# Kernel optimization log

Hardware: AMD Instinct MI355X
Metric: run time of the kernel (lower is better)

Reference implementation:

```python
import jax, jax.numpy as jnp
import numpy as np

B = 65536
QUERY_DIM = 1024
CROSS_DIM = 1024
HEADS = 16
DIM_HEAD = 64
INNER = HEADS * DIM_HEAD  # 1024
SCALE = DIM_HEAD ** -0.5


def setup_inputs() -> dict:
    key = jax.random.key(0)
    ks = jax.random.split(key, 7)
    s_in = 1.0 / np.sqrt(QUERY_DIM)
    s_c = 1.0 / np.sqrt(CROSS_DIM)
    s_o = 1.0 / np.sqrt(INNER)
    return {
        "latent": jax.random.normal(ks[0], (B, QUERY_DIM), jnp.float32),
        "cond_latent": jax.random.normal(ks[1], (B, CROSS_DIM), jnp.float32),
        "Wq": jax.random.normal(ks[2], (INNER, QUERY_DIM), jnp.float32) * s_in,
        "Wk": jax.random.normal(ks[3], (INNER, CROSS_DIM), jnp.float32) * s_c,
        "Wv": jax.random.normal(ks[4], (INNER, CROSS_DIM), jnp.float32) * s_c,
        "Wout": jax.random.normal(ks[5], (QUERY_DIM, INNER), jnp.float32) * s_o,
        "bout": jax.random.normal(ks[6], (QUERY_DIM,), jnp.float32) * s_o,
    }


def reference(latent, cond_latent, Wq, Wk, Wv, Wout, bout):
    # projections: [B, inner] -> [B, heads, dim_head]
    Q = (latent @ Wq.T).reshape(B, HEADS, DIM_HEAD)
    K = (cond_latent @ Wk.T).reshape(B, HEADS, DIM_HEAD)
    V = (cond_latent @ Wv.T).reshape(B, HEADS, DIM_HEAD)
    # attention across the heads axis: scores [B, heads, heads]
    scores = jnp.einsum("bhd,bgd->bhg", Q, K) * SCALE
    probs = jax.nn.softmax(scores, axis=-1)
    feats = jnp.einsum("bhg,bgd->bhd", probs, V).reshape(B, INNER)
    return feats @ Wout.T + bout
```

## Files before the change

### kernel.cpp

```cpp
#include <hip/hip_runtime.h>
#include <hip/hip_bf16.h>

#define NB    65536
#define KDIM  1024
#define NDIM  1024

#define BM 256
#define BN 256
#define BK 64
#define NT (KDIM / BK)

typedef float f32x4 __attribute__((ext_vector_type(4)));
typedef short short8 __attribute__((ext_vector_type(8)));
typedef unsigned short ushort8v __attribute__((ext_vector_type(8)));

static __device__ __forceinline__ unsigned short f2bf(float f) {
    union { float f; unsigned u; } v; v.f = f;
    unsigned r = v.u + 0x7FFFu + ((v.u >> 16) & 1u);
    return (unsigned short)(r >> 16);
}
static __device__ __forceinline__ float bf2f(unsigned short h) {
    union { unsigned u; float f; } v; v.u = ((unsigned)h) << 16;
    return v.f;
}

static __device__ __forceinline__ void gload16(const unsigned short* g, unsigned short* l) {
    __builtin_amdgcn_global_load_lds(
        (const __attribute__((address_space(1))) unsigned int*)g,
        (__attribute__((address_space(3))) unsigned int*)l, 16, 0, 0);
}

__global__ __launch_bounds__(256) void f32_to_bf16_k(
    const float* __restrict__ s, unsigned short* __restrict__ d, int n4)
{
    const int stride = gridDim.x * 256;
    for (int i = blockIdx.x * 256 + threadIdx.x; i < n4; i += stride) {
        float4 v = reinterpret_cast<const float4*>(s)[i];
        ushort4 o;
        o.x = f2bf(v.x); o.y = f2bf(v.y); o.z = f2bf(v.z); o.w = f2bf(v.w);
        reinterpret_cast<ushort4*>(d)[i] = o;
    }
}

template<int OUT_F32>
__global__ __launch_bounds__(512, 2) void gemm256(
    const unsigned short* __restrict__ Ap, const unsigned short* __restrict__ Wp,
    const float* __restrict__ bias, void* __restrict__ Cptr)
{
    constexpr int N = NDIM;
    constexpr int GN = NDIM / BN;
    __shared__ alignas(16) unsigned short lds[2][2][32][512];

    const int t    = threadIdx.x;
    const int lane = t & 63;
    const int wid  = t >> 6;
    const int wm   = wid >> 2;
    const int wn   = wid & 3;

    const int nwg  = gridDim.x;
    const int cpx  = nwg >> 3;
    const int orig = blockIdx.x;
    const int wgid = (orig & 7) * cpx + (orig >> 3);
    const int bn0  = (wgid & (GN - 1)) * BN;
    const int bm0  = (wgid / GN) * BM;

    const size_t aoff = (size_t)(lane & 15) * KDIM + (lane >> 4) * 8;

#define FENCE_ asm volatile("" ::: "memory")
#define BAR_   do { FENCE_; __builtin_amdgcn_s_barrier(); FENCE_; } while (0)
#define VMBAR_ do { asm volatile("s_waitcnt vmcnt(8)" ::: "memory");            \
                    __builtin_amdgcn_s_barrier(); FENCE_; } while (0)

#define LDA_(BUF, MI, KS) \
    (*reinterpret_cast<const short8*>(&lds[BUF][0][(wm * 8 + (MI)) * 2 + (KS)][lane * 8]))
#define LDB_(BUF, NI, KS) \
    (*reinterpret_cast<const short8*>(&lds[BUF][1][(wn * 4 + (NI)) * 2 + (KS)][lane * 8]))

#define STAGE_(TAU, SLOT, AB, KS) do {                                          \
        int _tc = (TAU) < NT ? (TAU) : NT - 1;    \
        const unsigned short* _b = (AB) ? Wp : Ap;                              \
        int _r0 = (AB) ? bn0 : bm0;                                             \
        _Pragma("unroll")                                                       \
        for (int _j = 0; _j < 2; ++_j) {                                        \
            int _f = wid * 2 + _j;                                              \
            gload16(_b + (size_t)(_r0 + _f * 16) * KDIM + _tc * BK + (KS) * 32 + aoff, \
                    &lds[SLOT][AB][_f * 2 + (KS)][0]);                          \
        }                                                                       \
    } while (0)

#define MFMA_(ACCB, AF) do { _Pragma("unroll")                                  \
    for (int mi = 0; mi < 4; ++mi) {                                            \
        acc[(ACCB) + mi][0] = __builtin_amdgcn_mfma_f32_16x16x32_bf16(AF[mi], bq0, acc[(ACCB) + mi][0], 0, 0, 0); \
        acc[(ACCB) + mi][1] = __builtin_amdgcn_mfma_f32_16x16x32_bf16(AF[mi], bq1, acc[(ACCB) + mi][1], 0, 0, 0); \
        acc[(ACCB) + mi][2] = __builtin_amdgcn_mfma_f32_16x16x32_bf16(AF[mi], bq2, acc[(ACCB) + mi][2], 0, 0, 0); \
        acc[(ACCB) + mi][3] = __builtin_amdgcn_mfma_f32_16x16x32_bf16(AF[mi], bq3, acc[(ACCB) + mi][3], 0, 0, 0); \
    } } while (0)

#define GROUP_(BUF, OBUF, TT) do {                                              \
                                                   \
        _Pragma("unroll")                                                       \
        for (int mi = 0; mi < 4; ++mi) afA[mi] = LDA_(BUF, mi, 0);              \
        bq0 = LDB_(BUF, 0, 0); bq1 = LDB_(BUF, 1, 0);                           \
        bq2 = LDB_(BUF, 2, 0); bq3 = LDB_(BUF, 3, 0);                           \
        STAGE_((TT) + 1, OBUF, 0, 1);                                           \
        BAR_;                                                                   \
        __builtin_amdgcn_s_setprio(1); MFMA_(0, afA); __builtin_amdgcn_s_setprio(0); \
        BAR_;                                                                   \
                                                   \
        _Pragma("unroll")                                                       \
        for (int mi = 0; mi < 4; ++mi) afB[mi] = LDA_(BUF, 4 + mi, 0);          \
        STAGE_((TT) + 1, OBUF, 1, 1);                                           \
        VMBAR_;                                                                 \
        __builtin_amdgcn_s_setprio(1); MFMA_(4, afB); __builtin_amdgcn_s_setprio(0); \
        BAR_;                                                                   \
                                                   \
        _Pragma("unroll")                                                       \
        for (int mi = 0; mi < 4; ++mi) afA[mi] = LDA_(BUF, mi, 1);              \
        bq0 = LDB_(BUF, 0, 1); bq1 = LDB_(BUF, 1, 1);                           \
        bq2 = LDB_(BUF, 2, 1); bq3 = LDB_(BUF, 3, 1);                           \
        STAGE_((TT) + 2, BUF, 0, 0);                                            \
        BAR_;                                                                   \
        __builtin_amdgcn_s_setprio(1); MFMA_(0, afA); __builtin_amdgcn_s_setprio(0); \
        BAR_;                                                                   \
                                                   \
        _Pragma("unroll")                                                       \
        for (int mi = 0; mi < 4; ++mi) afB[mi] = LDA_(BUF, 4 + mi, 1);          \
        STAGE_((TT) + 2, BUF, 1, 0);                                            \
        VMBAR_;                                                                 \
        __builtin_amdgcn_s_setprio(1); MFMA_(4, afB); __builtin_amdgcn_s_setprio(0); \
        BAR_;                                                                   \
    } while (0)

    f32x4 acc[8][4];
#pragma unroll
    for (int mi = 0; mi < 8; ++mi)
#pragma unroll
        for (int ni = 0; ni < 4; ++ni)
            acc[mi][ni] = (f32x4){0.f, 0.f, 0.f, 0.f};

    short8 afA[4], afB[4], bq0, bq1, bq2, bq3;

    STAGE_(0, 0, 0, 0); STAGE_(0, 0, 1, 0);
    STAGE_(0, 0, 0, 1); STAGE_(0, 0, 1, 1);
    STAGE_(1, 1, 0, 0); STAGE_(1, 1, 1, 0);
    VMBAR_;

#pragma unroll 1
    for (int tt = 0; tt < NT; tt += 2) {
        GROUP_(0, 1, tt);
        GROUP_(1, 0, tt + 1);
    }

    asm volatile("s_waitcnt vmcnt(0)" ::: "memory");

    const int crow = (lane >> 4) * 4;
    const int ccol = lane & 15;
    if (OUT_F32) {
        float* Cf = (float*)Cptr;
        float bv[4];
#pragma unroll
        for (int ni = 0; ni < 4; ++ni)
            bv[ni] = bias[bn0 + wn * 64 + ni * 16 + ccol];
#pragma unroll
        for (int mi = 0; mi < 8; ++mi)
#pragma unroll
            for (int ni = 0; ni < 4; ++ni) {
                size_t base = (size_t)(bm0 + wm * 128 + mi * 16 + crow) * N
                            + (bn0 + wn * 64 + ni * 16 + ccol);
#pragma unroll
                for (int r = 0; r < 4; ++r)
                    Cf[base + (size_t)r * N] = acc[mi][ni][r] + bv[ni];
            }
    } else {
        unsigned short* Cb = (unsigned short*)Cptr;
#pragma unroll
        for (int mi = 0; mi < 8; ++mi)
#pragma unroll
            for (int ni = 0; ni < 4; ++ni) {
                size_t base = (size_t)(bm0 + wm * 128 + mi * 16 + crow) * N
                            + (bn0 + wn * 64 + ni * 16 + ccol);
#pragma unroll
                for (int r = 0; r < 4; ++r)
                    Cb[base + (size_t)r * N] = f2bf(acc[mi][ni][r]);
            }
    }
#undef FENCE_
#undef BAR_
#undef VMBAR_
#undef LDA_
#undef LDB_
#undef STAGE_
#undef MFMA_
#undef GROUP_
}

__global__ __launch_bounds__(256) void attn_k(
    const unsigned short* __restrict__ Qb, const unsigned short* __restrict__ Kb,
    const unsigned short* __restrict__ Vb, unsigned short* __restrict__ Fb)
{
    __shared__ alignas(16) unsigned short KL[4][1024];
    __shared__ alignas(16) unsigned short VL[4][1024];
    const int t = threadIdx.x;
    const int lane = t & 63;
    const int wid = t >> 6;
    const size_t row = (size_t)blockIdx.x * 4 + wid;
    const size_t base = row * 1024;
    const int off = lane * 16;

    ushort8v q0 = *reinterpret_cast<const ushort8v*>(&Qb[base + off]);
    ushort8v q1 = *reinterpret_cast<const ushort8v*>(&Qb[base + off + 8]);
    float qf[16];
#pragma unroll
    for (int j = 0; j < 8; ++j) { qf[j] = bf2f(q0[j]); qf[8 + j] = bf2f(q1[j]); }

    *reinterpret_cast<ushort8v*>(&KL[wid][off])     = *reinterpret_cast<const ushort8v*>(&Kb[base + off]);
    *reinterpret_cast<ushort8v*>(&KL[wid][off + 8]) = *reinterpret_cast<const ushort8v*>(&Kb[base + off + 8]);
    *reinterpret_cast<ushort8v*>(&VL[wid][off])     = *reinterpret_cast<const ushort8v*>(&Vb[base + off]);
    *reinterpret_cast<ushort8v*>(&VL[wid][off + 8]) = *reinterpret_cast<const ushort8v*>(&Vb[base + off + 8]);
    __syncthreads();

    const int sub = lane & 3;
    float s[16];
#pragma unroll
    for (int g = 0; g < 16; ++g) {
        const ushort8v k0 = *reinterpret_cast<const ushort8v*>(&KL[wid][g * 64 + sub * 16]);
        const ushort8v k1 = *reinterpret_cast<const ushort8v*>(&KL[wid][g * 64 + sub * 16 + 8]);
        float acc = 0.f;
#pragma unroll
        for (int j = 0; j < 8; ++j)
            acc += qf[j] * bf2f(k0[j]) + qf[8 + j] * bf2f(k1[j]);
        s[g] = acc;
    }
#pragma unroll
    for (int m = 1; m <= 2; m <<= 1)
#pragma unroll
        for (int g = 0; g < 16; ++g)
            s[g] += __shfl_xor(s[g], m, 64);

    float mx = s[0];
#pragma unroll
    for (int g = 1; g < 16; ++g) mx = fmaxf(mx, s[g]);
    float p[16], denom = 0.f;
#pragma unroll
    for (int g = 0; g < 16; ++g) {
        p[g] = __expf((s[g] - mx) * 0.125f);
        denom += p[g];
    }
    float inv = 1.f / denom;

    float f[16];
#pragma unroll
    for (int j = 0; j < 16; ++j) f[j] = 0.f;
#pragma unroll
    for (int g = 0; g < 16; ++g) {
        float pg = p[g] * inv;
        const ushort8v v0 = *reinterpret_cast<const ushort8v*>(&VL[wid][g * 64 + sub * 16]);
        const ushort8v v1 = *reinterpret_cast<const ushort8v*>(&VL[wid][g * 64 + sub * 16 + 8]);
#pragma unroll
        for (int j = 0; j < 8; ++j) {
            f[j]     += pg * bf2f(v0[j]);
            f[8 + j] += pg * bf2f(v1[j]);
        }
    }
    ushort8v o0, o1;
#pragma unroll
    for (int j = 0; j < 8; ++j) { o0[j] = f2bf(f[j]); o1[j] = f2bf(f[8 + j]); }
    *reinterpret_cast<ushort8v*>(&Fb[base + off])     = o0;
    *reinterpret_cast<ushort8v*>(&Fb[base + off + 8]) = o1;
}

extern "C" void kernel_launch(void* const* d_in, const int* in_sizes, int n_in,
                              void* d_out, int out_size, void* d_ws, size_t ws_size,
                              hipStream_t stream)
{
    (void)in_sizes; (void)n_in; (void)out_size; (void)ws_size;
    const float* latent = (const float*)d_in[0];
    const float* cond   = (const float*)d_in[1];
    const float* Wq     = (const float*)d_in[2];
    const float* Wk     = (const float*)d_in[3];
    const float* Wv     = (const float*)d_in[4];
    const float* Wout   = (const float*)d_in[5];
    const float* bout   = (const float*)d_in[6];
    float* out = (float*)d_out;

    char* ws = (char*)d_ws;
    const size_t MB = 1ull << 20;
    unsigned short* wqb = (unsigned short*)(ws + 0 * MB);
    unsigned short* wkb = (unsigned short*)(ws + 2 * MB);
    unsigned short* wvb = (unsigned short*)(ws + 4 * MB);
    unsigned short* wob = (unsigned short*)(ws + 6 * MB);
    unsigned short* Qb  = (unsigned short*)(ws + 8 * MB);
    unsigned short* Kbf = (unsigned short*)(ws + 8 * MB + 128 * MB);
    unsigned short* Vbf = (unsigned short*)(ws + 8 * MB + 256 * MB);
    unsigned short* Lb  = (unsigned short*)(ws + 8 * MB + 384 * MB);
    unsigned short* Cb  = (unsigned short*)(ws + 8 * MB + 512 * MB);

    const int wn4 = (KDIM * NDIM) / 4;
    f32_to_bf16_k<<<1024, 256, 0, stream>>>(Wq,   wqb, wn4);
    f32_to_bf16_k<<<1024, 256, 0, stream>>>(Wk,   wkb, wn4);
    f32_to_bf16_k<<<1024, 256, 0, stream>>>(Wv,   wvb, wn4);
    f32_to_bf16_k<<<1024, 256, 0, stream>>>(Wout, wob, wn4);

    const int an4 = (NB * KDIM) / 4;
    f32_to_bf16_k<<<4096, 256, 0, stream>>>(latent, Lb, an4);
    f32_to_bf16_k<<<4096, 256, 0, stream>>>(cond,   Cb, an4);

    const int nblk = (NB / BM) * (NDIM / BN);
    gemm256<0><<<nblk, 512, 0, stream>>>(Lb, wqb, nullptr, Qb);
    gemm256<0><<<nblk, 512, 0, stream>>>(Cb, wkb, nullptr, Kbf);
    gemm256<0><<<nblk, 512, 0, stream>>>(Cb, wvb, nullptr, Vbf);

    attn_k<<<NB / 4, 256, 0, stream>>>(Qb, Kbf, Vbf, Qb);

    gemm256<1><<<nblk, 512, 0, stream>>>(Qb, wob, bout, out);
}
```

Before: 1.015 ms.

## Simplify GEMM main loop to one-tile prefetch and stage epilogue through LDS

Replaces the finely interleaved half-tile staging schedule, with its partial vmcnt waits and many barriers, with a simple double-buffered loop. Each iteration prefetches the whole next K tile, runs all 64 MFMAs per warp, then waits for all loads and takes one barrier. The epilogue now goes through LDS in row bands so global stores become wide coalesced vector writes instead of scattered scalar writes. The cost is less overlap of loads with compute, since vmcnt(0) sits at the end of every iteration, plus extra LDS traffic and syncthreads in the epilogue.

```diff
diff --git a/kernel.cpp b/kernel.cpp
--- a/kernel.cpp
+++ b/kernel.cpp
@@ -49,7 +49,7 @@
 {
     constexpr int N = NDIM;
     constexpr int GN = NDIM / BN;
-    __shared__ alignas(16) unsigned short lds[2][2][32][512];
+    __shared__ alignas(16) unsigned short lds[2][2][16][1024];
 
     const int t    = threadIdx.x;
     const int lane = t & 63;
@@ -66,71 +66,28 @@
 
     const size_t aoff = (size_t)(lane & 15) * KDIM + (lane >> 4) * 8;
 
-#define FENCE_ asm volatile("" ::: "memory")
-#define BAR_   do { FENCE_; __builtin_amdgcn_s_barrier(); FENCE_; } while (0)
-#define VMBAR_ do { asm volatile("s_waitcnt vmcnt(8)" ::: "memory");            \
-                    __builtin_amdgcn_s_barrier(); FENCE_; } while (0)
-
 #define LDA_(BUF, MI, KS) \
-    (*reinterpret_cast<const short8*>(&lds[BUF][0][(wm * 8 + (MI)) * 2 + (KS)][lane * 8]))
+    (*reinterpret_cast<const short8*>(&lds[BUF][0][wm * 8 + (MI)][(KS) * 512 + lane * 8]))
 #define LDB_(BUF, NI, KS) \
-    (*reinterpret_cast<const short8*>(&lds[BUF][1][(wn * 4 + (NI)) * 2 + (KS)][lane * 8]))
-
-#define STAGE_(TAU, SLOT, AB, KS) do {                                          \
-        int _tc = (TAU) < NT ? (TAU) : NT - 1;    \
-        const unsigned short* _b = (AB) ? Wp : Ap;                              \
-        int _r0 = (AB) ? bn0 : bm0;                                             \
+    (*reinterpret_cast<const short8*>(&lds[BUF][1][wn * 4 + (NI)][(KS) * 512 + lane * 8]))
+
+#define STAGE_(TAU, SLOT) do {                                                  \
         _Pragma("unroll")                                                       \
-        for (int _j = 0; _j < 2; ++_j) {                                        \
-            int _f = wid * 2 + _j;                                              \
-            gload16(_b + (size_t)(_r0 + _f * 16) * KDIM + _tc * BK + (KS) * 32 + aoff, \
-                    &lds[SLOT][AB][_f * 2 + (KS)][0]);                          \
+        for (int _ab = 0; _ab < 2; ++_ab) {                                     \
+            const unsigned short* _b = _ab ? Wp : Ap;                           \
+            int _r0 = _ab ? bn0 : bm0;                                          \
+            _Pragma("unroll")                                                   \
+            for (int _j = 0; _j < 2; ++_j) {                                    \
+                int _f = wid * 2 + _j;                                          \
+                _Pragma("unroll")                                               \
+                for (int _ks = 0; _ks < 2; ++_ks)                               \
+                    gload16(_b + (size_t)(_r0 + _f * 16) * KDIM                 \
+                                + (TAU) * BK + _ks * 32 + aoff,                 \
+                            &lds[SLOT][_ab][_f][_ks * 512]);                    \
+            }                                                                   \
         }                                                                       \
     } while (0)
 
-#define MFMA_(ACCB, AF) do { _Pragma("unroll")                                  \
-    for (int mi = 0; mi < 4; ++mi) {                                            \
-        acc[(ACCB) + mi][0] = __builtin_amdgcn_mfma_f32_16x16x32_bf16(AF[mi], bq0, acc[(ACCB) + mi][0], 0, 0, 0); \
-        acc[(ACCB) + mi][1] = __builtin_amdgcn_mfma_f32_16x16x32_bf16(AF[mi], bq1, acc[(ACCB) + mi][1], 0, 0, 0); \
-        acc[(ACCB) + mi][2] = __builtin_amdgcn_mfma_f32_16x16x32_bf16(AF[mi], bq2, acc[(ACCB) + mi][2], 0, 0, 0); \
-        acc[(ACCB) + mi][3] = __builtin_amdgcn_mfma_f32_16x16x32_bf16(AF[mi], bq3, acc[(ACCB) + mi][3], 0, 0, 0); \
-    } } while (0)
-
-#define GROUP_(BUF, OBUF, TT) do {                                              \
-                                                   \
-        _Pragma("unroll")                                                       \
-        for (int mi = 0; mi < 4; ++mi) afA[mi] = LDA_(BUF, mi, 0);              \
-        bq0 = LDB_(BUF, 0, 0); bq1 = LDB_(BUF, 1, 0);                           \
-        bq2 = LDB_(BUF, 2, 0); bq3 = LDB_(BUF, 3, 0);                           \
-        STAGE_((TT) + 1, OBUF, 0, 1);                                           \
-        BAR_;                                                                   \
-        __builtin_amdgcn_s_setprio(1); MFMA_(0, afA); __builtin_amdgcn_s_setprio(0); \
-        BAR_;                                                                   \
-                                                   \
-        _Pragma("unroll")                                                       \
-        for (int mi = 0; mi < 4; ++mi) afB[mi] = LDA_(BUF, 4 + mi, 0);          \
-        STAGE_((TT) + 1, OBUF, 1, 1);                                           \
-        VMBAR_;                                                                 \
-        __builtin_amdgcn_s_setprio(1); MFMA_(4, afB); __builtin_amdgcn_s_setprio(0); \
-        BAR_;                                                                   \
-                                                   \
-        _Pragma("unroll")                                                       \
-        for (int mi = 0; mi < 4; ++mi) afA[mi] = LDA_(BUF, mi, 1);              \
-        bq0 = LDB_(BUF, 0, 1); bq1 = LDB_(BUF, 1, 1);                           \
-        bq2 = LDB_(BUF, 2, 1); bq3 = LDB_(BUF, 3, 1);                           \
-        STAGE_((TT) + 2, BUF, 0, 0);                                            \
-        BAR_;                                                                   \
-        __builtin_amdgcn_s_setprio(1); MFMA_(0, afA); __builtin_amdgcn_s_setprio(0); \
-        BAR_;                                                                   \
-                                                   \
-        _Pragma("unroll")                                                       \
-        for (int mi = 0; mi < 4; ++mi) afB[mi] = LDA_(BUF, 4 + mi, 1);          \
-        STAGE_((TT) + 2, BUF, 1, 0);                                            \
-        VMBAR_;                                                                 \
-        __builtin_amdgcn_s_setprio(1); MFMA_(4, afB); __builtin_amdgcn_s_setprio(0); \
-        BAR_;                                                                   \
-    } while (0)
-
     f32x4 acc[8][4];
 #pragma unroll
     for (int mi = 0; mi < 8; ++mi)
@@ -138,60 +95,97 @@
         for (int ni = 0; ni < 4; ++ni)
             acc[mi][ni] = (f32x4){0.f, 0.f, 0.f, 0.f};
 
-    short8 afA[4], afB[4], bq0, bq1, bq2, bq3;
-
-    STAGE_(0, 0, 0, 0); STAGE_(0, 0, 1, 0);
-    STAGE_(0, 0, 0, 1); STAGE_(0, 0, 1, 1);
-    STAGE_(1, 1, 0, 0); STAGE_(1, 1, 1, 0);
-    VMBAR_;
+    STAGE_(0, 0);
+    asm volatile("s_waitcnt vmcnt(0)" ::: "memory");
+    __builtin_amdgcn_s_barrier();
 
 #pragma unroll 1
-    for (int tt = 0; tt < NT; tt += 2) {
-        GROUP_(0, 1, tt);
-        GROUP_(1, 0, tt + 1);
-    }
-
-    asm volatile("s_waitcnt vmcnt(0)" ::: "memory");
+    for (int tt = 0; tt < NT; ++tt) {
+        const int buf = tt & 1;
+        if (tt + 1 < NT) STAGE_(tt + 1, buf ^ 1);
+
+#pragma unroll
+        for (int ks = 0; ks < 2; ++ks) {
+            short8 af[8], bq[4];
+#pragma unroll
+            for (int mi = 0; mi < 8; ++mi) af[mi] = LDA_(buf, mi, ks);
+#pragma unroll
+            for (int ni = 0; ni < 4; ++ni) bq[ni] = LDB_(buf, ni, ks);
+            __builtin_amdgcn_s_setprio(1);
+#pragma unroll
+            for (int mi = 0; mi < 8; ++mi)
+#pragma unroll
+                for (int ni = 0; ni < 4; ++ni)
+                    acc[mi][ni] = __builtin_amdgcn_mfma_f32_16x16x32_bf16(
+                        af[mi], bq[ni], acc[mi][ni], 0, 0, 0);
+            __builtin_amdgcn_s_setprio(0);
+        }
+        asm volatile("s_waitcnt vmcnt(0)" ::: "memory");
+        __builtin_amdgcn_s_barrier();
+    }
 
     const int crow = (lane >> 4) * 4;
     const int ccol = lane & 15;
+
     if (OUT_F32) {
         float* Cf = (float*)Cptr;
+        float* bbf = reinterpret_cast<float*>(&lds[0][0][0][0]);
         float bv[4];
 #pragma unroll
         for (int ni = 0; ni < 4; ++ni)
             bv[ni] = bias[bn0 + wn * 64 + ni * 16 + ccol];
 #pragma unroll
-        for (int mi = 0; mi < 8; ++mi)
-#pragma unroll
-            for (int ni = 0; ni < 4; ++ni) {
-                size_t base = (size_t)(bm0 + wm * 128 + mi * 16 + crow) * N
-                            + (bn0 + wn * 64 + ni * 16 + ccol);
-#pragma unroll
-                for (int r = 0; r < 4; ++r)
-                    Cf[base + (size_t)r * N] = acc[mi][ni][r] + bv[ni];
+        for (int p = 0; p < 8; ++p) {
+            if (wm == (p >> 2)) {
+#pragma unroll
+                for (int ml = 0; ml < 2; ++ml)
+#pragma unroll
+                    for (int ni = 0; ni < 4; ++ni)
+#pragma unroll
+                        for (int r = 0; r < 4; ++r)
+                            bbf[(ml * 16 + crow + r) * 268 + wn * 64 + ni * 16 + ccol]
+                                = acc[(p & 3) * 2 + ml][ni][r] + bv[ni];
             }
+            __syncthreads();
+#pragma unroll
+            for (int it = 0; it < 4; ++it) {
+                int lrow = wid * 4 + it;
+                f32x4 v = *reinterpret_cast<const f32x4*>(&bbf[lrow * 268 + lane * 4]);
+                *reinterpret_cast<f32x4*>(
+                    &Cf[(size_t)(bm0 + p * 32 + lrow) * N + bn0 + lane * 4]) = v;
+            }
+            __syncthreads();
+        }
     } else {
         unsigned short* Cb = (unsigned short*)Cptr;
-#pragma unroll
-        for (int mi = 0; mi < 8; ++mi)
-#pragma unroll
-            for (int ni = 0; ni < 4; ++ni) {
-                size_t base = (size_t)(bm0 + wm * 128 + mi * 16 + crow) * N
-                            + (bn0 + wn * 64 + ni * 16 + ccol);
-#pragma unroll
-                for (int r = 0; r < 4; ++r)
-                    Cb[base + (size_t)r * N] = f2bf(acc[mi][ni][r]);
+        unsigned short* bb = &lds[0][0][0][0];
+#pragma unroll
+        for (int p = 0; p < 4; ++p) {
+            if (wm == (p >> 1)) {
+#pragma unroll
+                for (int ml = 0; ml < 4; ++ml)
+#pragma unroll
+                    for (int ni = 0; ni < 4; ++ni)
+#pragma unroll
+                        for (int r = 0; r < 4; ++r)
+                            bb[(ml * 16 + crow + r) * 264 + wn * 64 + ni * 16 + ccol]
+                                = f2bf(acc[(p & 1) * 4 + ml][ni][r]);
             }
-    }
-#undef FENCE_
-#undef BAR_
-#undef VMBAR_
+            __syncthreads();
+#pragma unroll
+            for (int it = 0; it < 4; ++it) {
+                int lrow = wid * 8 + it * 2 + (lane >> 5);
+                int lcol = (lane & 31) * 8;
+                ushort8v v = *reinterpret_cast<const ushort8v*>(&bb[lrow * 264 + lcol]);
+                *reinterpret_cast<ushort8v*>(
+                    &Cb[(size_t)(bm0 + p * 64 + lrow) * N + bn0 + lcol]) = v;
+            }
+            __syncthreads();
+        }
+    }
 #undef LDA_
 #undef LDB_
 #undef STAGE_
-#undef MFMA_
-#undef GROUP_
 }
 
 __global__ __launch_bounds__(256) void attn_k(
```

Measured after the change: 1.069 ms. +5.3%, slower.
